# Kernel tuning notes

Hardware: AMD Instinct MI355X
Metric: run time of the kernel (lower is better)

Reference implementation:

```python
import jax, jax.numpy as jnp
import numpy as np
from jax import lax

B, T, I, H, L = 64, 256, 512, 1024, 2


def setup_inputs() -> dict:
    key = jax.random.key(0)
    ks = jax.random.split(key, 6)
    s = 0.05  # small init scale for numerical stability
    return {
        "x": jax.random.normal(ks[0], (B, T, I), dtype=jnp.float32),
        "h0": jnp.zeros((L, B, H), dtype=jnp.float32),
        "c0": jnp.zeros((L, B, H), dtype=jnp.float32),
        "W_ih_0": jax.random.normal(ks[1], (I, 4 * H), dtype=jnp.float32) * s,
        "W_hh_0": jax.random.normal(ks[2], (H, 4 * H), dtype=jnp.float32) * s,
        "b_0": jnp.zeros((4 * H,), dtype=jnp.float32),
        "W_ih_1": jax.random.normal(ks[3], (H, 4 * H), dtype=jnp.float32) * s,
        "W_hh_1": jax.random.normal(ks[4], (H, 4 * H), dtype=jnp.float32) * s,
        "b_1": jnp.zeros((4 * H,), dtype=jnp.float32),
    }


def _lstm_layer(x_tbd, h0, c0, W_ih, W_hh, b):
    """x_tbd: [T, B, in]; returns ([T, B, H], h_T, c_T). Standard (Zaremba) LSTM cell."""
    def step(carry, xt):
        h, c = carry
        gates = xt @ W_ih + h @ W_hh + b  # [B, 4H]
        i, f, g, o = jnp.split(gates, 4, axis=-1)
        i = jax.nn.sigmoid(i)
        f = jax.nn.sigmoid(f)
        g = jnp.tanh(g)
        o = jax.nn.sigmoid(o)
        c_new = f * c + i * g
        h_new = o * jnp.tanh(c_new)
        return (h_new, c_new), h_new

    (h_T, c_T), ys = lax.scan(step, (h0, c0), x_tbd)
    return ys, h_T, c_T


def reference(x, h0, c0, W_ih_0, W_hh_0, b_0, W_ih_1, W_hh_1, b_1):
    # x: [B, T, I] batch-first as in the torch module; scan over time.
    xt = jnp.swapaxes(x, 0, 1)  # [T, B, I]
    weights = [(W_ih_0, W_hh_0, b_0), (W_ih_1, W_hh_1, b_1)]
    hs, cs = [], []
    values = xt
    for l in range(L):
        W_ih, W_hh, b = weights[l]
        values, h_T, c_T = _lstm_layer(values, h0[l], c0[l], W_ih, W_hh, b)
        hs.append(h_T)
        cs.append(c_T)
    outputs = jnp.swapaxes(values, 0, 1)  # [B, T, H]
    return outputs, jnp.stack(hs, 0), jnp.stack(cs, 0)
```

## Files before the change

### kernel.cpp

```cpp
#include <hip/hip_runtime.h>
#include <hip/hip_bf16.h>

typedef __attribute__((ext_vector_type(8))) short short8;
typedef __attribute__((ext_vector_type(4))) float f32x4;
typedef __attribute__((ext_vector_type(2))) int int2v;

constexpr int BB = 64;
constexpr int TT = 256;
constexpr int II = 512;
constexpr int HH = 1024;

constexpr int NBLK = 256;
constexpr int NTHR = 512;

constexpr int HTILE = (HH / 8) * BB * 8;
constexpr int XTILE = (II / 8) * BB * 8;
constexpr int RING = 8;

constexpr size_t OFF_FLAGS = 0;
constexpr size_t OFF_WIH0T = 4096;
constexpr size_t OFF_WHH0T = OFF_WIH0T + (size_t)4096 * 512 * 2;
constexpr size_t OFF_WIH1T = OFF_WHH0T + (size_t)4096 * 1024 * 2;
constexpr size_t OFF_WHH1T = OFF_WIH1T + (size_t)4096 * 1024 * 2;
constexpr size_t OFF_XT    = OFF_WHH1T + (size_t)4096 * 1024 * 2;
constexpr size_t OFF_H0D   = OFF_XT + (size_t)TT * XTILE * 2;
constexpr size_t OFF_H1D   = OFF_H0D + (size_t)RING * HTILE * 2;

__device__ __forceinline__ float sigmoid_(float x) {
  return 1.f / (1.f + __expf(-x));
}
__device__ __forceinline__ float tanh_(float x) {
  float ax = fabsf(x);
  float e = __expf(-2.f * ax);
  float t = (1.f - e) / (1.f + e);
  return copysignf(t, x);
}

__global__ void zero_flags(int* f) { f[blockIdx.x * 256 + threadIdx.x] = 0; }

__global__ void transpose_to_bf16(const float* __restrict__ src,
                                  __hip_bfloat16* __restrict__ dst,
                                  int K, int N) {
  __shared__ float tile[64][65];
  const int n0 = blockIdx.x * 64;
  const int k0 = blockIdx.y * 64;
  const int tx = threadIdx.x & 63;
  const int ty = threadIdx.x >> 6;
#pragma unroll
  for (int i = 0; i < 64; i += 4)
    tile[ty + i][tx] = src[(size_t)(k0 + ty + i) * N + n0 + tx];
  __syncthreads();
#pragma unroll
  for (int i = 0; i < 64; i += 4) {
    const int n = ty + i;
    dst[(size_t)(n0 + n) * K + k0 + tx] = __float2bfloat16(tile[tx][n]);
  }
}

__global__ void tile_x(const float* __restrict__ x, __hip_bfloat16* __restrict__ xt) {
  const int t = blockIdx.x;
  const int k = threadIdx.x;
  __hip_bfloat16* o = xt + (size_t)t * XTILE;
  for (int b = 0; b < BB; ++b) {
    float v = x[((size_t)b * TT + t) * II + k];
    o[(k >> 3) * (BB * 8) + b * 8 + (k & 7)] = __float2bfloat16(v);
  }
}

__global__ void init_h(const float* __restrict__ h0, __hip_bfloat16* h0d, __hip_bfloat16* h1d) {
  const int idx = blockIdx.x * 256 + threadIdx.x;
  const int l = idx >> 16;
  const int b = (idx >> 10) & 63;
  const int j = idx & 1023;
  __hip_bfloat16 v = __float2bfloat16(h0[idx]);
  __hip_bfloat16* dst = l ? h1d : h0d;
  dst[(j >> 3) * (BB * 8) + b * 8 + (j & 7)] = v;
}

template <int LAYER>
__device__ __forceinline__ int chunk_kg(int wave, int c) {
  if constexpr (LAYER == 0)
    return (c < 2) ? (wave * 2 + c) * 32 : 512 + (wave * 4 + (c - 2)) * 32;
  else
    return (c < 4) ? (wave * 4 + c) * 32 : 1024 + (wave * 4 + (c - 4)) * 32;
}

template <int KI, int KW, int CA, int LAYER>
__device__ __forceinline__ void scan_impl(
    const __hip_bfloat16* __restrict__ xsrc,
    const __hip_bfloat16* __restrict__ WiT,
    const __hip_bfloat16* __restrict__ WhT,
    const float* __restrict__ bias,
    const float* __restrict__ c0_in,
    __hip_bfloat16* h0d, __hip_bfloat16* h1d,
    float* __restrict__ out, int* flags, f32x4 (*part)[2][4][64],
    int bhalf, int jbase, int fslot) {
  const int tid = threadIdx.x;
  const int wave = tid >> 6;
  const int lane = tid & 63;
  const int cc = lane & 15;
  const int lrow = lane >> 4;
  constexpr int NB = KW - CA;

  short8 Bf[KW][4];
#pragma unroll
  for (int c = 0; c < KW; ++c) {
    const int kg = chunk_kg<LAYER>(wave, c) + lrow * 8;
#pragma unroll
    for (int g = 0; g < 4; ++g) {
      const int gcol = g * HH + jbase + cc;
      const __hip_bfloat16* p;
      if (kg < KI) p = WiT + (size_t)gcol * KI + kg;
      else         p = WhT + (size_t)gcol * HH + (kg - KI);
      Bf[c][g] = *(const short8*)p;
    }
  }

  const int ejl = tid & 15;
  const int ebl = tid >> 4;
  const int ej = jbase + ejl;
  const int eb = bhalf * 32 + ebl;
  const int pm = ebl >> 4, psub = (ebl >> 2) & 3, pr = ebl & 3;
  const int rdbase = pm * 1024 + (psub * 16 + ejl) * 4 + pr;
  const float bi = bias[ej];
  const float bf_ = bias[HH + ej];
  const float bg = bias[2 * HH + ej];
  const float bo = bias[3 * HH + ej];
  float cst = c0_in[(size_t)LAYER * BB * HH + (size_t)eb * HH + ej];

  const int* fpair = flags + bhalf * 128 + lane * 2;

  for (int tau = 0; tau < TT + 2; ++tau) {
    const bool active = (LAYER == 0) ? (tau < TT) : (tau >= 2);
    const int p = (LAYER == 0) ? tau : tau - 2;

    const __hip_bfloat16* px;
    const __hip_bfloat16* ph;
    __hip_bfloat16* hout;
    if constexpr (LAYER == 0) {
      px = xsrc + (size_t)p * XTILE;
      ph = h0d + (size_t)(p & (RING - 1)) * HTILE;
      hout = h0d + (size_t)((p + 1) & (RING - 1)) * HTILE;
    } else {
      px = h0d + (size_t)((p + 1) & (RING - 1)) * HTILE;
      ph = h1d + (size_t)(p & (RING - 1)) * HTILE;
      hout = h1d + (size_t)((p + 1) & (RING - 1)) * HTILE;
    }

    f32x4 acc[2][4] = {};
    short8 abuf[4][2];

    auto issue_chunk = [&](int c, short8* dst) {
      const int kg = chunk_kg<LAYER>(wave, c);
      const __hip_bfloat16* ab;
      int kc;
      if (kg < KI) { ab = px; kc = (kg >> 3) + lrow; }
      else         { ab = ph; kc = ((kg - KI) >> 3) + lrow; }
#pragma unroll
      for (int m = 0; m < 2; ++m) {
        const __hip_bfloat16* ptr =
            ab + (size_t)kc * (BB * 8) + (size_t)(bhalf * 32 + m * 16 + cc) * 8;
        asm volatile("global_load_dwordx4 %0, %1, off" : "=v"(dst[m]) : "v"(ptr));
      }
    };

    if (active) {
#pragma unroll
      for (int c = 0; c < CA; ++c) issue_chunk(c, abuf[c]);
    }

    if (tau > 0 && wave == 0) {
      for (;;) {
        int2v v;
        asm volatile("global_load_dwordx2 %0, %1, off sc0 sc1\n\t"
                     "s_waitcnt vmcnt(0)"
                     : "=v"(v) : "v"(fpair) : "memory");
        int mn = min(v.x, v.y);
        if (__all(mn >= tau)) break;
        __builtin_amdgcn_s_sleep(2);
      }
    }

    if (active) {
      asm volatile("s_waitcnt vmcnt(0)" ::: "memory");
      __builtin_amdgcn_sched_barrier(0);
#pragma unroll
      for (int c = 0; c < CA; ++c)
#pragma unroll
        for (int m = 0; m < 2; ++m)
#pragma unroll
          for (int g = 0; g < 4; ++g)
            acc[m][g] = __builtin_amdgcn_mfma_f32_16x16x32_bf16(
                abuf[c][m], Bf[c][g], acc[m][g], 0, 0, 0);
    }

    if (tau > 0 && wave == 0)
      __builtin_amdgcn_fence(__ATOMIC_ACQUIRE, "agent");
    __syncthreads();

    if (active) {
#pragma unroll
      for (int c = 0; c < NB; ++c) issue_chunk(CA + c, abuf[c]);
#pragma unroll
      for (int c = 0; c < NB; ++c) {
        const int vm = 2 * (NB - 1 - c);
        if (vm == 6)      asm volatile("s_waitcnt vmcnt(6)" ::: "memory");
        else if (vm == 4) asm volatile("s_waitcnt vmcnt(4)" ::: "memory");
        else if (vm == 2) asm volatile("s_waitcnt vmcnt(2)" ::: "memory");
        else              asm volatile("s_waitcnt vmcnt(0)" ::: "memory");
        __builtin_amdgcn_sched_barrier(0);
#pragma unroll
        for (int m = 0; m < 2; ++m)
#pragma unroll
          for (int g = 0; g < 4; ++g)
            acc[m][g] = __builtin_amdgcn_mfma_f32_16x16x32_bf16(
                abuf[c][m], Bf[CA + c][g], acc[m][g], 0, 0, 0);
      }

#pragma unroll
      for (int m = 0; m < 2; ++m)
#pragma unroll
        for (int g = 0; g < 4; ++g)
          part[wave][m][g][lane] = acc[m][g];
      __syncthreads();

      const float* pp = (const float*)part;
      float s0 = 0.f, s1 = 0.f, s2 = 0.f, s3 = 0.f;
#pragma unroll
      for (int w = 0; w < 8; ++w) {
        s0 += pp[w * 2048 + 0 * 256 + rdbase];
        s1 += pp[w * 2048 + 1 * 256 + rdbase];
        s2 += pp[w * 2048 + 2 * 256 + rdbase];
        s3 += pp[w * 2048 + 3 * 256 + rdbase];
      }
      float iv = sigmoid_(s0 + bi);
      float fv = sigmoid_(s1 + bf_);
      float gv = tanh_(s2 + bg);
      float ov = sigmoid_(s3 + bo);
      float cn = fv * cst + iv * gv;
      cst = cn;
      float hv = ov * tanh_(cn);
      __hip_bfloat16 hb = __float2bfloat16(hv);
      unsigned short hu = *reinterpret_cast<unsigned short*>(&hb);
      unsigned pu = (unsigned)__shfl_xor((int)hu, 1);
      if ((tid & 1) == 0) {
        uint32_t packed = (uint32_t)hu | ((pu & 0xffffu) << 16);
        uint32_t* hq = (uint32_t*)hout;
        __hip_atomic_store(hq + (ej >> 3) * 256 + eb * 4 + ((ej & 7) >> 1), packed,
                           __ATOMIC_RELAXED, __HIP_MEMORY_SCOPE_AGENT);
      }
      asm volatile("s_waitcnt vmcnt(0)" ::: "memory");
      __syncthreads();
      if (tid == 0)
        __hip_atomic_store(&flags[fslot], tau + 1, __ATOMIC_RELAXED, __HIP_MEMORY_SCOPE_AGENT);
      if constexpr (LAYER == 1)
        out[((size_t)eb * TT + p) * HH + ej] = hv;
      if (p == TT - 1) {
        out[(size_t)BB * TT * HH + (size_t)LAYER * BB * HH + (size_t)eb * HH + ej] = hv;
        out[(size_t)BB * TT * HH + (size_t)2 * BB * HH + (size_t)LAYER * BB * HH + (size_t)eb * HH + ej] = cn;
      }
      asm volatile("s_waitcnt vmcnt(0)" ::: "memory");
    } else {
      if (tid == 0)
        __hip_atomic_store(&flags[fslot], tau + 1, __ATOMIC_RELAXED, __HIP_MEMORY_SCOPE_AGENT);
    }
  }
}

__global__ __launch_bounds__(NTHR, 2) void lstm_scan(
    const __hip_bfloat16* __restrict__ xt,
    const __hip_bfloat16* __restrict__ Wih0T, const __hip_bfloat16* __restrict__ Whh0T,
    const __hip_bfloat16* __restrict__ Wih1T, const __hip_bfloat16* __restrict__ Whh1T,
    const float* __restrict__ b0, const float* __restrict__ b1,
    const float* __restrict__ c0_in,
    __hip_bfloat16* h0d, __hip_bfloat16* h1d,
    float* __restrict__ out, int* flags) {
  __shared__ f32x4 part[8][2][4][64];
  const int blk = blockIdx.x;
  const int jslot = blk & 63;
  const int bhalf = (blk >> 6) & 1;
  const int layer = blk >> 7;
  const int jbase = jslot * 16;
  const int fslot = bhalf * 128 + layer * 64 + jslot;
  if (layer == 0)
    scan_impl<512, 6, 2, 0>(xt, Wih0T, Whh0T, b0, c0_in, h0d, h1d, out, flags, part, bhalf, jbase, fslot);
  else
    scan_impl<1024, 8, 4, 1>(nullptr, Wih1T, Whh1T, b1, c0_in, h0d, h1d, out, flags, part, bhalf, jbase, fslot);
}

extern "C" void kernel_launch(void* const* d_in, const int* in_sizes, int n_in,
                              void* d_out, int out_size, void* d_ws, size_t ws_size,
                              hipStream_t stream) {
  (void)in_sizes; (void)n_in; (void)out_size; (void)ws_size;
  const float* x    = (const float*)d_in[0];
  const float* h0   = (const float*)d_in[1];
  const float* c0   = (const float*)d_in[2];
  const float* Wih0 = (const float*)d_in[3];
  const float* Whh0 = (const float*)d_in[4];
  const float* b0   = (const float*)d_in[5];
  const float* Wih1 = (const float*)d_in[6];
  const float* Whh1 = (const float*)d_in[7];
  const float* b1   = (const float*)d_in[8];
  float* out = (float*)d_out;
  char* ws = (char*)d_ws;

  int* flags = (int*)(ws + OFF_FLAGS);
  __hip_bfloat16* wih0t = (__hip_bfloat16*)(ws + OFF_WIH0T);
  __hip_bfloat16* whh0t = (__hip_bfloat16*)(ws + OFF_WHH0T);
  __hip_bfloat16* wih1t = (__hip_bfloat16*)(ws + OFF_WIH1T);
  __hip_bfloat16* whh1t = (__hip_bfloat16*)(ws + OFF_WHH1T);
  __hip_bfloat16* xtl   = (__hip_bfloat16*)(ws + OFF_XT);
  __hip_bfloat16* h0d   = (__hip_bfloat16*)(ws + OFF_H0D);
  __hip_bfloat16* h1d   = (__hip_bfloat16*)(ws + OFF_H1D);

  zero_flags<<<2, 256, 0, stream>>>(flags);
  transpose_to_bf16<<<dim3(64, 8),  256, 0, stream>>>(Wih0, wih0t, 512, 4096);
  transpose_to_bf16<<<dim3(64, 16), 256, 0, stream>>>(Whh0, whh0t, 1024, 4096);
  transpose_to_bf16<<<dim3(64, 16), 256, 0, stream>>>(Wih1, wih1t, 1024, 4096);
  transpose_to_bf16<<<dim3(64, 16), 256, 0, stream>>>(Whh1, whh1t, 1024, 4096);
  tile_x<<<TT, 512, 0, stream>>>(x, xtl);
  init_h<<<512, 256, 0, stream>>>(h0, h0d, h1d);
  lstm_scan<<<NBLK, NTHR, 0, stream>>>(xtl, wih0t, whh0t, wih1t, whh1t,
                                       b0, b1, c0, h0d, h1d, out, flags);
}
```

Before: 1.521 ms.

## Relax layer-0 wait on layer-1 and defer wave-0 early MFMAs past barrier

The flag slot layout is interleaved so each lane's flag pair holds the layer-0 and layer-1 progress for the same column slot. Layer 0 now waits on layer 1 with a slack of 5 steps instead of 0, so it can run further ahead within the 8-entry ring. Wave 0, which does the polling, skips the early MFMA phase and runs those MFMAs after the barrier, overlapped with its second-chunk loads. The acquire fence moves to the top of the loop. The goal is less time spent on the critical path of the cross-block handshake, at the risk of ring-buffer overwrite hazards if the slack is too large and a heavier load on wave 0 after the barrier.

```diff
diff --git a/kernel.cpp b/kernel.cpp
--- a/kernel.cpp
+++ b/kernel.cpp
@@ -134,6 +134,9 @@
     const bool active = (LAYER == 0) ? (tau < TT) : (tau >= 2);
     const int p = (LAYER == 0) ? tau : tau - 2;
 
+    if (tau > 0 && wave == 0)
+      __builtin_amdgcn_fence(__ATOMIC_ACQUIRE, "agent");
+
     const __hip_bfloat16* px;
     const __hip_bfloat16* ph;
     __hip_bfloat16* hout;
@@ -148,7 +151,8 @@
     }
 
     f32x4 acc[2][4] = {};
-    short8 abuf[4][2];
+    short8 abufA[CA][2];
+    short8 abufB[NB][2];
 
     auto issue_chunk = [&](int c, short8* dst) {
       const int kg = chunk_kg<LAYER>(wave, c);
@@ -166,7 +170,7 @@
 
     if (active) {
 #pragma unroll
-      for (int c = 0; c < CA; ++c) issue_chunk(c, abuf[c]);
+      for (int c = 0; c < CA; ++c) issue_chunk(c, abufA[c]);
     }
 
     if (tau > 0 && wave == 0) {
@@ -175,13 +179,15 @@
         asm volatile("global_load_dwordx2 %0, %1, off sc0 sc1\n\t"
                      "s_waitcnt vmcnt(0)"
                      : "=v"(v) : "v"(fpair) : "memory");
-        int mn = min(v.x, v.y);
+        int mn;
+        if constexpr (LAYER == 0) mn = min(v.x, v.y + 5);
+        else                      mn = min(v.x, v.y);
         if (__all(mn >= tau)) break;
         __builtin_amdgcn_s_sleep(2);
       }
     }
 
-    if (active) {
+    if (active && wave != 0) {
       asm volatile("s_waitcnt vmcnt(0)" ::: "memory");
       __builtin_amdgcn_sched_barrier(0);
 #pragma unroll
@@ -191,16 +197,28 @@
 #pragma unroll
           for (int g = 0; g < 4; ++g)
             acc[m][g] = __builtin_amdgcn_mfma_f32_16x16x32_bf16(
-                abuf[c][m], Bf[c][g], acc[m][g], 0, 0, 0);
-    }
-
-    if (tau > 0 && wave == 0)
-      __builtin_amdgcn_fence(__ATOMIC_ACQUIRE, "agent");
+                abufA[c][m], Bf[c][g], acc[m][g], 0, 0, 0);
+    }
+
     __syncthreads();
 
     if (active) {
 #pragma unroll
-      for (int c = 0; c < NB; ++c) issue_chunk(CA + c, abuf[c]);
+      for (int c = 0; c < NB; ++c) issue_chunk(CA + c, abufB[c]);
+
+      if (wave == 0) {
+        asm volatile("s_waitcnt vmcnt(8)" ::: "memory");
+        __builtin_amdgcn_sched_barrier(0);
+#pragma unroll
+        for (int c = 0; c < CA; ++c)
+#pragma unroll
+          for (int m = 0; m < 2; ++m)
+#pragma unroll
+            for (int g = 0; g < 4; ++g)
+              acc[m][g] = __builtin_amdgcn_mfma_f32_16x16x32_bf16(
+                  abufA[c][m], Bf[c][g], acc[m][g], 0, 0, 0);
+      }
+
 #pragma unroll
       for (int c = 0; c < NB; ++c) {
         const int vm = 2 * (NB - 1 - c);
@@ -214,7 +232,7 @@
 #pragma unroll
           for (int g = 0; g < 4; ++g)
             acc[m][g] = __builtin_amdgcn_mfma_f32_16x16x32_bf16(
-                abuf[c][m], Bf[CA + c][g], acc[m][g], 0, 0, 0);
+                abufB[c][m], Bf[CA + c][g], acc[m][g], 0, 0, 0);
       }
 
 #pragma unroll
@@ -281,7 +299,7 @@
   const int bhalf = (blk >> 6) & 1;
   const int layer = blk >> 7;
   const int jbase = jslot * 16;
-  const int fslot = bhalf * 128 + layer * 64 + jslot;
+  const int fslot = bhalf * 128 + jslot * 2 + layer;
   if (layer == 0)
     scan_impl<512, 6, 2, 0>(xt, Wih0T, Whh0T, b0, c0_in, h0d, h1d, out, flags, part, bhalf, jbase, fslot);
   else
```

Result: slower. 1.756 ms (+15.4%).
